# Kernel optimization log

Hardware: AMD Instinct MI355X
Metric: run time of the kernel (lower is better)

Reference implementation:

```python
import jax, jax.numpy as jnp
import numpy as np

B, C, H, W = 8, 512, 32, 32
N_HEADS = 4
D_K = C // N_HEADS  # 128


def setup_inputs() -> dict:
    key = jax.random.key(0)
    k1, k2, k3, k4, k5 = jax.random.split(key, 5)
    x = jax.random.normal(k1, (B, C, H, W), dtype=jnp.float32)
    # projection: Linear(in_ch, n_heads*d_k*3)
    Wp = jax.random.normal(k2, (C, N_HEADS * D_K * 3), dtype=jnp.float32) * (C ** -0.5)
    bp = jax.random.normal(k3, (N_HEADS * D_K * 3,), dtype=jnp.float32) * 0.01
    # output: Linear(n_heads*d_k, in_ch)
    Wo = jax.random.normal(k4, (N_HEADS * D_K, C), dtype=jnp.float32) * ((N_HEADS * D_K) ** -0.5)
    bo = jax.random.normal(k5, (C,), dtype=jnp.float32) * 0.01
    return {"x": x, "Wp": Wp, "bp": bp, "Wo": Wo, "bo": bo}


def reference(x, Wp, bp, Wo, bo):
    b, c, h, w = x.shape
    scale = D_K ** -0.5
    # [B, C, H, W] -> [B, N, C], N = H*W
    xs = x.reshape(b, c, h * w).transpose(0, 2, 1)
    qkv = (xs @ Wp + bp).reshape(b, h * w, N_HEADS, 3 * D_K)
    q, k, v = jnp.split(qkv, 3, axis=-1)  # each [B, N, H, D]
    attn = jnp.einsum('bihd,bjhd->bijh', q, k) * scale
    attn = jax.nn.softmax(attn, axis=2)  # softmax over j (keys)
    out = jnp.einsum('bijh,bjhd->bihd', attn, v)
    out = out.reshape(b, h * w, N_HEADS * D_K)
    out = out @ Wo + bo
    out = out + xs  # residual (note: GroupNorm is unused in the original forward)
    return out.transpose(0, 2, 1).reshape(b, c, h, w)
```

## Files before the change

### kernel.cpp

```cpp
#include <hip/hip_runtime.h>

#define NB 8
#define NC 512
#define NTOK 1024
#define NHEADS 4
#define DKH 128

typedef unsigned short u16;
typedef __attribute__((ext_vector_type(8))) short bf16x8;
typedef __attribute__((ext_vector_type(4))) float f32x4;

__device__ inline u16 f2b(float f) {
    union { float f; unsigned u; } v; v.f = f;
    unsigned r = v.u + 0x7fffu + ((v.u >> 16) & 1u);
    return (u16)(r >> 16);
}

__device__ __forceinline__ void gll16(const u16* g, u16* l) {
    __builtin_amdgcn_global_load_lds((const __attribute__((address_space(1))) unsigned*)g,
                                     (__attribute__((address_space(3))) unsigned*)l, 16, 0, 0);
}

__global__ __launch_bounds__(256) void prep(const float* __restrict__ x, const float* __restrict__ Wp,
                                            const float* __restrict__ Wo,
                                            u16* __restrict__ xsb, u16* __restrict__ WpT, u16* __restrict__ WoT)
{
    __shared__ float tile[32][33];
    const int z = blockIdx.z;
    const float* src; u16* dst; int R, Cc;
    if (z == 0)      { src = Wp; dst = WpT; R = 512; Cc = 1536; }
    else if (z == 1) { if (blockIdx.x >= 16) return; src = Wo; dst = WoT; R = 512; Cc = 512; }
    else             { if (blockIdx.x >= 32) return;
                       src = x + (long)(z-2)*NC*NTOK; dst = xsb + (long)(z-2)*NTOK*NC; R = NC; Cc = NTOK; }
    int c0 = blockIdx.x * 32, r0 = blockIdx.y * 32;
    int tx = threadIdx.x, ty = threadIdx.y;
    #pragma unroll
    for (int k = 0; k < 4; ++k)
        tile[ty + 8*k][tx] = src[(long)(r0 + ty + 8*k) * Cc + c0 + tx];
    __syncthreads();
    #pragma unroll
    for (int k = 0; k < 4; ++k)
        dst[(long)(c0 + ty + 8*k) * R + r0 + tx] = f2b(tile[tx][ty + 8*k]);
}

__global__ __launch_bounds__(256) void gemm_qkv(const u16* __restrict__ WpT, const u16* __restrict__ xsb,
                                                const float* __restrict__ bp,
                                                u16* __restrict__ qg, u16* __restrict__ kg, u16* __restrict__ vg)
{
    __shared__ union SmU {
        struct { u16 As[128][64]; u16 Bs[128][64]; } s;
        u16 Os[4][64][72];
    } sm;
    const int tid = threadIdx.x;
    const int m0 = blockIdx.x * 128;
    const int n0 = blockIdx.y * 128;
    const int w = tid >> 6, lane = tid & 63, quad = lane >> 4, lc = lane & 15;
    const int mo = (w & 1) * 64, no = (w >> 1) * 64;
    const int sw8 = (((lane & 7) ^ (lane >> 3)) << 3);
    const int xs = lc & 7;

    f32x4 acc[4][4] = {};

    for (int k0 = 0; k0 < NC; k0 += 64) {
        __syncthreads();
        #pragma unroll
        for (int p = 0; p < 4; ++p) {
            int row = w*32 + p*8 + (lane >> 3);
            gll16(&WpT[(long)(m0 + row) * NC + k0 + sw8], &sm.s.As[w*32 + p*8][0]);
            gll16(&xsb[(long)(n0 + row) * NC + k0 + sw8], &sm.s.Bs[w*32 + p*8][0]);
        }
        __syncthreads();
        #pragma unroll
        for (int ks = 0; ks < 2; ++ks) {
            bf16x8 af[4], bfr[4];
            #pragma unroll
            for (int t = 0; t < 4; ++t) {
                af[t]  = *(const bf16x8*)&sm.s.As[mo + t*16 + lc][((ks*4 + quad) ^ xs) << 3];
                bfr[t] = *(const bf16x8*)&sm.s.Bs[no + t*16 + lc][((ks*4 + quad) ^ xs) << 3];
            }
            #pragma unroll
            for (int mt = 0; mt < 4; ++mt)
                #pragma unroll
                for (int nt = 0; nt < 4; ++nt)
                    acc[mt][nt] = __builtin_amdgcn_mfma_f32_16x16x32_bf16(af[mt], bfr[nt], acc[mt][nt], 0, 0, 0);
        }
    }
    __syncthreads();

    const int bb = n0 >> 10;
    const int nblk = n0 & 1023;
    const int cqb = m0 + mo;
    const int h = cqb / 384;
    const int rem = cqb - h * 384;
    const int sel = rem >> 7;
    const int d_base = rem & 127;

    #pragma unroll
    for (int mt = 0; mt < 4; ++mt) {
        int cq0 = cqb + mt*16 + quad*4;
        float b0 = bp[cq0+0], b1 = bp[cq0+1], b2 = bp[cq0+2], b3 = bp[cq0+3];
        #pragma unroll
        for (int nt = 0; nt < 4; ++nt) {
            f32x4 a = acc[mt][nt];
            int nl = nt*16 + lc;
            int ml = mt*16 + quad*4;
            u16 e0 = f2b(a[0]+b0), e1 = f2b(a[1]+b1), e2 = f2b(a[2]+b2), e3 = f2b(a[3]+b3);
            if (sel == 2) {
                sm.Os[w][ml+0][nl] = e0; sm.Os[w][ml+1][nl] = e1;
                sm.Os[w][ml+2][nl] = e2; sm.Os[w][ml+3][nl] = e3;
            } else {
                sm.Os[w][nl][ml+0] = e0; sm.Os[w][nl][ml+1] = e1;
                sm.Os[w][nl][ml+2] = e2; sm.Os[w][nl][ml+3] = e3;
            }
        }
    }
    __builtin_amdgcn_sched_barrier(0);

    const long bhbase = (long)(bb * NHEADS + h);
    const int sw = sw8;
    if (sel == 2) {
        #pragma unroll
        for (int pass = 0; pass < 8; ++pass) {
            int ml  = pass*8 + (lane >> 3);
            int nl0 = (lane & 7) * 8;
            bf16x8 vv = *(const bf16x8*)&sm.Os[w][ml][nl0];
            *(bf16x8*)&vg[((bhbase*DKH + d_base + ml) << 10) + nblk + no + sw] = vv;
        }
    } else if (sel == 1) {
        #pragma unroll
        for (int pass = 0; pass < 8; ++pass) {
            int nl  = pass*8 + (lane >> 3);
            int ml0 = (lane & 7) * 8;
            bf16x8 vv = *(const bf16x8*)&sm.Os[w][nl][ml0];
            *(bf16x8*)&kg[((bhbase*NTOK + nblk + no + nl) << 7) + d_base + sw] = vv;
        }
    } else {
        #pragma unroll
        for (int pass = 0; pass < 8; ++pass) {
            int nl  = pass*8 + (lane >> 3);
            int ml0 = (lane & 7) * 8;
            bf16x8 vv = *(const bf16x8*)&sm.Os[w][nl][ml0];
            *(bf16x8*)&qg[((bhbase*NTOK + nblk + no + nl) << 7) + d_base + ml0] = vv;
        }
    }
}

__global__ __launch_bounds__(512) void attn(const u16* __restrict__ qg, const u16* __restrict__ kg,
                                            const u16* __restrict__ vtg, u16* __restrict__ ho)
{
    __shared__ u16 Ks[2][64*128];
    __shared__ u16 Vt[2][128*64];
    __shared__ u16 Ps[8][16][72];
    const int tid = threadIdx.x;
    const int w = tid >> 6, lane = tid & 63, quad = lane >> 4, lc = lane & 15;
    const int id = blockIdx.x;
    const int xcd = id & 7, rest = id >> 3, sub = rest & 3, bx = rest >> 2;
    const int pr = xcd + sub*8;
    const int b = pr >> 2, h = pr & 3;
    const int i0 = bx*128 + w*16;
    const long bh = (long)(b * NHEADS + h) << 17;
    const u16* qb = qg + bh;
    const u16* kb = kg + bh;
    const u16* vb = vtg + bh;
    const float SL2E = 0.08838834764831845f * 1.4426950408889634f;

    bf16x8 qf[4];
    #pragma unroll
    for (int ks = 0; ks < 4; ++ks)
        qf[ks] = *(const bf16x8*)&qb[(long)(i0 + lc) * DKH + ks*32 + quad*8];

    f32x4 o[8] = {};
    float lsum = 0.f;
    const int xs = lc & 7;

    #pragma unroll
    for (int p = 0; p < 2; ++p) {
        int ck = (w*2 + p)*64 + lane;
        gll16(&kb[(long)ck * 8], &Ks[0][(w*2 + p)*512]);
        gll16(&vb[(((long)(ck >> 3)) << 10) + (ck & 7)*8], &Vt[0][(w*2 + p)*512]);
    }

    for (int t = 0; t < 16; ++t) {
        __syncthreads();
        if (t < 15) {
            long jo = (long)(t+1) * 64;
            #pragma unroll
            for (int p = 0; p < 2; ++p) {
                int ck = (w*2 + p)*64 + lane;
                gll16(&kb[jo*128 + (long)ck*8], &Ks[(t+1)&1][(w*2 + p)*512]);
                gll16(&vb[(((long)(ck >> 3)) << 10) + jo + (ck & 7)*8], &Vt[(t+1)&1][(w*2 + p)*512]);
            }
        }
        const u16* K = Ks[t&1];
        const u16* V = Vt[t&1];

        f32x4 s[4] = {};
        #pragma unroll
        for (int ks = 0; ks < 4; ++ks)
            #pragma unroll
            for (int jt = 0; jt < 4; ++jt) {
                bf16x8 kf = *(const bf16x8*)&K[(jt*16 + lc)*128 + (((ks*4 + quad) ^ xs) << 3)];
                s[jt] = __builtin_amdgcn_mfma_f32_16x16x32_bf16(kf, qf[ks], s[jt], 0, 0, 0);
            }

        #pragma unroll
        for (int jt = 0; jt < 4; ++jt) {
            float p0 = __builtin_amdgcn_exp2f(s[jt][0] * SL2E);
            float p1 = __builtin_amdgcn_exp2f(s[jt][1] * SL2E);
            float p2 = __builtin_amdgcn_exp2f(s[jt][2] * SL2E);
            float p3 = __builtin_amdgcn_exp2f(s[jt][3] * SL2E);
            lsum += (p0 + p1) + (p2 + p3);
            ushort4 pk;
            pk.x = f2b(p0); pk.y = f2b(p1); pk.z = f2b(p2); pk.w = f2b(p3);
            *(ushort4*)&Ps[w][lc][jt*16 + quad*4] = pk;
        }
        __builtin_amdgcn_sched_barrier(0);

        #pragma unroll
        for (int ks2 = 0; ks2 < 2; ++ks2) {
            bf16x8 pf = *(const bf16x8*)&Ps[w][lc][ks2*32 + quad*8];
            #pragma unroll
            for (int dt = 0; dt < 8; ++dt) {
                bf16x8 vf = *(const bf16x8*)&V[(dt*16 + lc)*64 + (((ks2*4 + quad) ^ xs) << 3)];
                o[dt] = __builtin_amdgcn_mfma_f32_16x16x32_bf16(vf, pf, o[dt], 0, 0, 0);
            }
        }
    }

    lsum += __shfl_xor(lsum, 16);
    lsum += __shfl_xor(lsum, 32);
    float inv = 1.0f / lsum;

    #pragma unroll
    for (int dt = 0; dt < 8; ++dt) {
        ushort4 pk;
        pk.x = f2b(o[dt][0] * inv); pk.y = f2b(o[dt][1] * inv);
        pk.z = f2b(o[dt][2] * inv); pk.w = f2b(o[dt][3] * inv);
        *(ushort4*)&ho[(long)(b*NTOK + i0 + lc) * NC + h*DKH + dt*16 + quad*4] = pk;
    }
}

__global__ __launch_bounds__(256) void gemm_out(const u16* __restrict__ WoT, const u16* __restrict__ ho,
                                                const float* __restrict__ bo, const float* __restrict__ xin,
                                                float* __restrict__ dout)
{
    __shared__ struct { u16 As[128][64]; u16 Bs[64][64]; } sm;
    const int tid = threadIdx.x;
    const int m0 = blockIdx.x * 128;
    const int n0 = blockIdx.y * 64;
    const int w = tid >> 6, lane = tid & 63, quad = lane >> 4, lc = lane & 15;
    const int mo = (w & 1) * 64, no = (w >> 1) * 32;
    const int sw8 = (((lane & 7) ^ (lane >> 3)) << 3);
    const int xs = lc & 7;

    f32x4 acc[4][2] = {};

    for (int k0 = 0; k0 < NC; k0 += 64) {
        __syncthreads();
        #pragma unroll
        for (int p = 0; p < 4; ++p) {
            int row = w*32 + p*8 + (lane >> 3);
            gll16(&WoT[(long)(m0 + row) * NC + k0 + sw8], &sm.As[w*32 + p*8][0]);
        }
        #pragma unroll
        for (int p = 0; p < 2; ++p) {
            int row = w*16 + p*8 + (lane >> 3);
            gll16(&ho[(long)(n0 + row) * NC + k0 + sw8], &sm.Bs[w*16 + p*8][0]);
        }
        __syncthreads();
        #pragma unroll
        for (int ks = 0; ks < 2; ++ks) {
            bf16x8 af[4], bfr[2];
            #pragma unroll
            for (int t = 0; t < 4; ++t)
                af[t] = *(const bf16x8*)&sm.As[mo + t*16 + lc][((ks*4 + quad) ^ xs) << 3];
            #pragma unroll
            for (int t = 0; t < 2; ++t)
                bfr[t] = *(const bf16x8*)&sm.Bs[no + t*16 + lc][((ks*4 + quad) ^ xs) << 3];
            #pragma unroll
            for (int mt = 0; mt < 4; ++mt)
                #pragma unroll
                for (int nt = 0; nt < 2; ++nt)
                    acc[mt][nt] = __builtin_amdgcn_mfma_f32_16x16x32_bf16(af[mt], bfr[nt], acc[mt][nt], 0, 0, 0);
        }
    }

    const int bb = n0 >> 10;
    #pragma unroll
    for (int mt = 0; mt < 4; ++mt) {
        int cc0 = m0 + mo + mt*16 + quad*4;
        float b0 = bo[cc0+0], b1 = bo[cc0+1], b2 = bo[cc0+2], b3 = bo[cc0+3];
        #pragma unroll
        for (int nt = 0; nt < 2; ++nt) {
            int nl = (n0 + no + nt*16 + lc) & (NTOK - 1);
            f32x4 a = acc[mt][nt];
            long ix = ((long)(bb*NC + cc0) << 10) + nl;
            dout[ix]             = a[0] + b0 + xin[ix];
            dout[ix + (1 << 10)] = a[1] + b1 + xin[ix + (1 << 10)];
            dout[ix + (2 << 10)] = a[2] + b2 + xin[ix + (2 << 10)];
            dout[ix + (3 << 10)] = a[3] + b3 + xin[ix + (3 << 10)];
        }
    }
}

extern "C" void kernel_launch(void* const* d_in, const int* in_sizes, int n_in,
                              void* d_out, int out_size, void* d_ws, size_t ws_size,
                              hipStream_t stream)
{
    (void)in_sizes; (void)n_in; (void)out_size; (void)ws_size;
    const float* x  = (const float*)d_in[0];
    const float* Wp = (const float*)d_in[1];
    const float* bp = (const float*)d_in[2];
    const float* Wo = (const float*)d_in[3];
    const float* bo = (const float*)d_in[4];
    float* out = (float*)d_out;

    u16* ws  = (u16*)d_ws;
    u16* xsb = ws;
    u16* WpT = xsb + (long)NB * NTOK * NC;
    u16* WoT = WpT + 1536L * 512;
    u16* qg  = WoT + 512L * 512;
    u16* kg  = qg + (long)NB * NHEADS * NTOK * DKH;
    u16* vtg = kg + (long)NB * NHEADS * NTOK * DKH;
    u16* ho  = vtg + (long)NB * NHEADS * NTOK * DKH;

    prep<<<dim3(48, 16, 10), dim3(32, 8), 0, stream>>>(x, Wp, Wo, xsb, WpT, WoT);
    gemm_qkv<<<dim3(1536/128, (NB*NTOK)/128), 256, 0, stream>>>(WpT, xsb, bp, qg, kg, vtg);
    attn<<<dim3(256), 512, 0, stream>>>(qg, kg, vtg, ho);
    gemm_out<<<dim3(NC/128, (NB*NTOK)/64), 256, 0, stream>>>(WoT, ho, bo, x, out);
}
```

Baseline: 140.2 us.

## Process two query tiles per wave in attention to reuse K/V fragments

Attention blocks drop from 8 to 4 waves, and each wave now handles 32 query rows (two 16-row tiles). Each K and V fragment read from LDS feeds two MFMAs, which halves LDS traffic per unit of compute. The P buffer gets an XOR swizzle in place of padding, and s_setprio raises wave priority around the MFMA sections. In exchange it uses more registers per wave, leaves fewer waves per block to hide latency, and with the grid unchanged gives fewer total waves.

```diff
diff --git a/kernel.cpp b/kernel.cpp
--- a/kernel.cpp
+++ b/kernel.cpp
@@ -145,39 +145,42 @@
     }
 }
 
-__global__ __launch_bounds__(512) void attn(const u16* __restrict__ qg, const u16* __restrict__ kg,
-                                            const u16* __restrict__ vtg, u16* __restrict__ ho)
+__global__ __launch_bounds__(256, 2) void attn(const u16* __restrict__ qg, const u16* __restrict__ kg,
+                                               const u16* __restrict__ vtg, u16* __restrict__ ho)
 {
     __shared__ u16 Ks[2][64*128];
     __shared__ u16 Vt[2][128*64];
-    __shared__ u16 Ps[8][16][72];
+    __shared__ u16 Ps[4][32][64];
     const int tid = threadIdx.x;
     const int w = tid >> 6, lane = tid & 63, quad = lane >> 4, lc = lane & 15;
     const int id = blockIdx.x;
     const int xcd = id & 7, rest = id >> 3, sub = rest & 3, bx = rest >> 2;
     const int pr = xcd + sub*8;
     const int b = pr >> 2, h = pr & 3;
-    const int i0 = bx*128 + w*16;
+    const int i0 = bx*128 + w*32;
     const long bh = (long)(b * NHEADS + h) << 17;
     const u16* qb = qg + bh;
     const u16* kb = kg + bh;
     const u16* vb = vtg + bh;
     const float SL2E = 0.08838834764831845f * 1.4426950408889634f;
 
-    bf16x8 qf[4];
-    #pragma unroll
-    for (int ks = 0; ks < 4; ++ks)
-        qf[ks] = *(const bf16x8*)&qb[(long)(i0 + lc) * DKH + ks*32 + quad*8];
-
-    f32x4 o[8] = {};
-    float lsum = 0.f;
+    bf16x8 qf[2][4];
+    #pragma unroll
+    for (int it = 0; it < 2; ++it)
+        #pragma unroll
+        for (int ks = 0; ks < 4; ++ks)
+            qf[it][ks] = *(const bf16x8*)&qb[(long)(i0 + it*16 + lc) * DKH + ks*32 + quad*8];
+
+    f32x4 o[2][8] = {};
+    float lsum0 = 0.f, lsum1 = 0.f;
     const int xs = lc & 7;
-
-    #pragma unroll
-    for (int p = 0; p < 2; ++p) {
-        int ck = (w*2 + p)*64 + lane;
-        gll16(&kb[(long)ck * 8], &Ks[0][(w*2 + p)*512]);
-        gll16(&vb[(((long)(ck >> 3)) << 10) + (ck & 7)*8], &Vt[0][(w*2 + p)*512]);
+    const int psw = (lc & 7) << 3;
+
+    #pragma unroll
+    for (int p = 0; p < 4; ++p) {
+        int ck = (w*4 + p)*64 + lane;
+        gll16(&kb[(long)ck * 8], &Ks[0][(w*4 + p)*512]);
+        gll16(&vb[(((long)(ck >> 3)) << 10) + (ck & 7)*8], &Vt[0][(w*4 + p)*512]);
     }
 
     for (int t = 0; t < 16; ++t) {
@@ -185,58 +188,75 @@
         if (t < 15) {
             long jo = (long)(t+1) * 64;
             #pragma unroll
-            for (int p = 0; p < 2; ++p) {
-                int ck = (w*2 + p)*64 + lane;
-                gll16(&kb[jo*128 + (long)ck*8], &Ks[(t+1)&1][(w*2 + p)*512]);
-                gll16(&vb[(((long)(ck >> 3)) << 10) + jo + (ck & 7)*8], &Vt[(t+1)&1][(w*2 + p)*512]);
+            for (int p = 0; p < 4; ++p) {
+                int ck = (w*4 + p)*64 + lane;
+                gll16(&kb[jo*128 + (long)ck*8], &Ks[(t+1)&1][(w*4 + p)*512]);
+                gll16(&vb[(((long)(ck >> 3)) << 10) + jo + (ck & 7)*8], &Vt[(t+1)&1][(w*4 + p)*512]);
             }
         }
         const u16* K = Ks[t&1];
         const u16* V = Vt[t&1];
 
-        f32x4 s[4] = {};
+        f32x4 s[2][4] = {};
+        __builtin_amdgcn_s_setprio(1);
         #pragma unroll
         for (int ks = 0; ks < 4; ++ks)
             #pragma unroll
             for (int jt = 0; jt < 4; ++jt) {
                 bf16x8 kf = *(const bf16x8*)&K[(jt*16 + lc)*128 + (((ks*4 + quad) ^ xs) << 3)];
-                s[jt] = __builtin_amdgcn_mfma_f32_16x16x32_bf16(kf, qf[ks], s[jt], 0, 0, 0);
-            }
-
-        #pragma unroll
-        for (int jt = 0; jt < 4; ++jt) {
-            float p0 = __builtin_amdgcn_exp2f(s[jt][0] * SL2E);
-            float p1 = __builtin_amdgcn_exp2f(s[jt][1] * SL2E);
-            float p2 = __builtin_amdgcn_exp2f(s[jt][2] * SL2E);
-            float p3 = __builtin_amdgcn_exp2f(s[jt][3] * SL2E);
-            lsum += (p0 + p1) + (p2 + p3);
-            ushort4 pk;
-            pk.x = f2b(p0); pk.y = f2b(p1); pk.z = f2b(p2); pk.w = f2b(p3);
-            *(ushort4*)&Ps[w][lc][jt*16 + quad*4] = pk;
-        }
+                s[0][jt] = __builtin_amdgcn_mfma_f32_16x16x32_bf16(kf, qf[0][ks], s[0][jt], 0, 0, 0);
+                s[1][jt] = __builtin_amdgcn_mfma_f32_16x16x32_bf16(kf, qf[1][ks], s[1][jt], 0, 0, 0);
+            }
+        __builtin_amdgcn_s_setprio(0);
+
+        #pragma unroll
+        for (int it = 0; it < 2; ++it)
+            #pragma unroll
+            for (int jt = 0; jt < 4; ++jt) {
+                float p0 = __builtin_amdgcn_exp2f(s[it][jt][0] * SL2E);
+                float p1 = __builtin_amdgcn_exp2f(s[it][jt][1] * SL2E);
+                float p2 = __builtin_amdgcn_exp2f(s[it][jt][2] * SL2E);
+                float p3 = __builtin_amdgcn_exp2f(s[it][jt][3] * SL2E);
+                if (it == 0) lsum0 += (p0 + p1) + (p2 + p3);
+                else         lsum1 += (p0 + p1) + (p2 + p3);
+                ushort4 pk;
+                pk.x = f2b(p0); pk.y = f2b(p1); pk.z = f2b(p2); pk.w = f2b(p3);
+                *(ushort4*)&Ps[w][it*16 + lc][(jt*16 + quad*4) ^ psw] = pk;
+            }
         __builtin_amdgcn_sched_barrier(0);
 
+        __builtin_amdgcn_s_setprio(1);
         #pragma unroll
         for (int ks2 = 0; ks2 < 2; ++ks2) {
-            bf16x8 pf = *(const bf16x8*)&Ps[w][lc][ks2*32 + quad*8];
+            bf16x8 pf0 = *(const bf16x8*)&Ps[w][lc]     [(ks2*32 + quad*8) ^ psw];
+            bf16x8 pf1 = *(const bf16x8*)&Ps[w][16 + lc][(ks2*32 + quad*8) ^ psw];
             #pragma unroll
             for (int dt = 0; dt < 8; ++dt) {
                 bf16x8 vf = *(const bf16x8*)&V[(dt*16 + lc)*64 + (((ks2*4 + quad) ^ xs) << 3)];
-                o[dt] = __builtin_amdgcn_mfma_f32_16x16x32_bf16(vf, pf, o[dt], 0, 0, 0);
-            }
-        }
-    }
-
-    lsum += __shfl_xor(lsum, 16);
-    lsum += __shfl_xor(lsum, 32);
-    float inv = 1.0f / lsum;
+                o[0][dt] = __builtin_amdgcn_mfma_f32_16x16x32_bf16(vf, pf0, o[0][dt], 0, 0, 0);
+                o[1][dt] = __builtin_amdgcn_mfma_f32_16x16x32_bf16(vf, pf1, o[1][dt], 0, 0, 0);
+            }
+        }
+        __builtin_amdgcn_s_setprio(0);
+    }
+
+    lsum0 += __shfl_xor(lsum0, 16);
+    lsum0 += __shfl_xor(lsum0, 32);
+    lsum1 += __shfl_xor(lsum1, 16);
+    lsum1 += __shfl_xor(lsum1, 32);
+    float inv0 = 1.0f / lsum0;
+    float inv1 = 1.0f / lsum1;
 
     #pragma unroll
     for (int dt = 0; dt < 8; ++dt) {
         ushort4 pk;
-        pk.x = f2b(o[dt][0] * inv); pk.y = f2b(o[dt][1] * inv);
-        pk.z = f2b(o[dt][2] * inv); pk.w = f2b(o[dt][3] * inv);
+        pk.x = f2b(o[0][dt][0] * inv0); pk.y = f2b(o[0][dt][1] * inv0);
+        pk.z = f2b(o[0][dt][2] * inv0); pk.w = f2b(o[0][dt][3] * inv0);
         *(ushort4*)&ho[(long)(b*NTOK + i0 + lc) * NC + h*DKH + dt*16 + quad*4] = pk;
+        ushort4 pk1;
+        pk1.x = f2b(o[1][dt][0] * inv1); pk1.y = f2b(o[1][dt][1] * inv1);
+        pk1.z = f2b(o[1][dt][2] * inv1); pk1.w = f2b(o[1][dt][3] * inv1);
+        *(ushort4*)&ho[(long)(b*NTOK + i0 + 16 + lc) * NC + h*DKH + dt*16 + quad*4] = pk1;
     }
 }
 
@@ -326,6 +346,6 @@
 
     prep<<<dim3(48, 16, 10), dim3(32, 8), 0, stream>>>(x, Wp, Wo, xsb, WpT, WoT);
     gemm_qkv<<<dim3(1536/128, (NB*NTOK)/128), 256, 0, stream>>>(WpT, xsb, bp, qg, kg, vtg);
-    attn<<<dim3(256), 512, 0, stream>>>(qg, kg, vtg, ho);
+    attn<<<dim3(256), 256, 0, stream>>>(qg, kg, vtg, ho);
     gemm_out<<<dim3(NC/128, (NB*NTOK)/64), 256, 0, stream>>>(WoT, ho, bo, x, out);
 }
```

Result: slower. 145.4 us (+3.7%).

## Enlarge QKV GEMM tiles to 256x256 with double-buffered LDS and XCD remap

Applied to the files above, without the earlier changes.

The QKV projection GEMM moves from 128x128 tiles with 256 threads to 256x256 tiles with 512 threads, so each wave computes 128x64 outputs. Global-to-LDS loads are now double-buffered, with vmcnt waits and raw barriers so the next K slice loads while the current one is multiplied, and MFMA sections raise wave priority. Block IDs are remapped across XCDs, and the epilogue writes Q, K and V in two 64-row halves. The goal is more operand reuse and hidden load latency. The cost is that only 192 blocks remain for the whole GPU, and 128KB of LDS limits each CU to one block.

```diff
diff --git a/kernel.cpp b/kernel.cpp
--- a/kernel.cpp
+++ b/kernel.cpp
@@ -43,105 +43,131 @@
         dst[(long)(c0 + ty + 8*k) * R + r0 + tx] = f2b(tile[tx][ty + 8*k]);
 }
 
-__global__ __launch_bounds__(256) void gemm_qkv(const u16* __restrict__ WpT, const u16* __restrict__ xsb,
-                                                const float* __restrict__ bp,
-                                                u16* __restrict__ qg, u16* __restrict__ kg, u16* __restrict__ vg)
+__global__ __launch_bounds__(512, 2) void gemm_qkv(const u16* __restrict__ WpT, const u16* __restrict__ xsb,
+                                                   const float* __restrict__ bp,
+                                                   u16* __restrict__ qg, u16* __restrict__ kg, u16* __restrict__ vg)
 {
     __shared__ union SmU {
-        struct { u16 As[128][64]; u16 Bs[128][64]; } s;
-        u16 Os[4][64][72];
+        struct { u16 As[2][256][64]; u16 Bs[2][256][64]; } s;
+        u16 Os[8][64][72];
     } sm;
     const int tid = threadIdx.x;
-    const int m0 = blockIdx.x * 128;
-    const int n0 = blockIdx.y * 128;
+    const int raw = blockIdx.x;
+    const int L = (raw & 7) * 24 + (raw >> 3);
+    const int mb = L % 6, nb = L / 6;
+    const int m0 = mb * 256;
+    const int n0 = nb * 256;
     const int w = tid >> 6, lane = tid & 63, quad = lane >> 4, lc = lane & 15;
-    const int mo = (w & 1) * 64, no = (w >> 1) * 64;
+    const int mo = (w & 1) * 128, no = (w >> 1) * 64;
     const int sw8 = (((lane & 7) ^ (lane >> 3)) << 3);
-    const int xs = lc & 7;
-
-    f32x4 acc[4][4] = {};
-
-    for (int k0 = 0; k0 < NC; k0 += 64) {
-        __syncthreads();
-        #pragma unroll
-        for (int p = 0; p < 4; ++p) {
-            int row = w*32 + p*8 + (lane >> 3);
-            gll16(&WpT[(long)(m0 + row) * NC + k0 + sw8], &sm.s.As[w*32 + p*8][0]);
-            gll16(&xsb[(long)(n0 + row) * NC + k0 + sw8], &sm.s.Bs[w*32 + p*8][0]);
-        }
-        __syncthreads();
+    const int xs = lc & 15 & 7;
+    const int srow = (lane >> 3);
+
+    f32x4 acc[8][4] = {};
+
+    #pragma unroll
+    for (int p = 0; p < 4; ++p) {
+        int row = w*32 + p*8 + srow;
+        gll16(&WpT[(long)(m0 + row) * NC + 0 + sw8], &sm.s.As[0][w*32 + p*8][0]);
+        gll16(&xsb[(long)(n0 + row) * NC + 0 + sw8], &sm.s.Bs[0][w*32 + p*8][0]);
+    }
+
+    for (int t = 0; t < 8; ++t) {
+        if (t < 7) {
+            const long kk = (long)(t + 1) * 64;
+            const int nbuf = (t + 1) & 1;
+            #pragma unroll
+            for (int p = 0; p < 4; ++p) {
+                int row = w*32 + p*8 + srow;
+                gll16(&WpT[(long)(m0 + row) * NC + kk + sw8], &sm.s.As[nbuf][w*32 + p*8][0]);
+                gll16(&xsb[(long)(n0 + row) * NC + kk + sw8], &sm.s.Bs[nbuf][w*32 + p*8][0]);
+            }
+            asm volatile("s_waitcnt vmcnt(8)" ::: "memory");
+        } else {
+            asm volatile("s_waitcnt vmcnt(0)" ::: "memory");
+        }
+        __builtin_amdgcn_s_barrier();
+        __builtin_amdgcn_sched_barrier(0);
+
+        const int cb = t & 1;
         #pragma unroll
         for (int ks = 0; ks < 2; ++ks) {
-            bf16x8 af[4], bfr[4];
-            #pragma unroll
-            for (int t = 0; t < 4; ++t) {
-                af[t]  = *(const bf16x8*)&sm.s.As[mo + t*16 + lc][((ks*4 + quad) ^ xs) << 3];
-                bfr[t] = *(const bf16x8*)&sm.s.Bs[no + t*16 + lc][((ks*4 + quad) ^ xs) << 3];
-            }
-            #pragma unroll
-            for (int mt = 0; mt < 4; ++mt)
+            bf16x8 af[8], bfr[4];
+            #pragma unroll
+            for (int mt = 0; mt < 8; ++mt)
+                af[mt] = *(const bf16x8*)&sm.s.As[cb][mo + mt*16 + lc][((ks*4 + quad) ^ xs) << 3];
+            #pragma unroll
+            for (int nt = 0; nt < 4; ++nt)
+                bfr[nt] = *(const bf16x8*)&sm.s.Bs[cb][no + nt*16 + lc][((ks*4 + quad) ^ xs) << 3];
+            __builtin_amdgcn_s_setprio(1);
+            #pragma unroll
+            for (int mt = 0; mt < 8; ++mt)
                 #pragma unroll
                 for (int nt = 0; nt < 4; ++nt)
                     acc[mt][nt] = __builtin_amdgcn_mfma_f32_16x16x32_bf16(af[mt], bfr[nt], acc[mt][nt], 0, 0, 0);
-        }
-    }
-    __syncthreads();
+            __builtin_amdgcn_s_setprio(0);
+        }
+        __builtin_amdgcn_s_barrier();
+    }
 
     const int bb = n0 >> 10;
     const int nblk = n0 & 1023;
-    const int cqb = m0 + mo;
-    const int h = cqb / 384;
-    const int rem = cqb - h * 384;
-    const int sel = rem >> 7;
-    const int d_base = rem & 127;
-
-    #pragma unroll
-    for (int mt = 0; mt < 4; ++mt) {
-        int cq0 = cqb + mt*16 + quad*4;
-        float b0 = bp[cq0+0], b1 = bp[cq0+1], b2 = bp[cq0+2], b3 = bp[cq0+3];
-        #pragma unroll
-        for (int nt = 0; nt < 4; ++nt) {
-            f32x4 a = acc[mt][nt];
-            int nl = nt*16 + lc;
-            int ml = mt*16 + quad*4;
-            u16 e0 = f2b(a[0]+b0), e1 = f2b(a[1]+b1), e2 = f2b(a[2]+b2), e3 = f2b(a[3]+b3);
-            if (sel == 2) {
-                sm.Os[w][ml+0][nl] = e0; sm.Os[w][ml+1][nl] = e1;
-                sm.Os[w][ml+2][nl] = e2; sm.Os[w][ml+3][nl] = e3;
-            } else {
-                sm.Os[w][nl][ml+0] = e0; sm.Os[w][nl][ml+1] = e1;
-                sm.Os[w][nl][ml+2] = e2; sm.Os[w][nl][ml+3] = e3;
-            }
-        }
-    }
-    __builtin_amdgcn_sched_barrier(0);
-
+    const int pb = (m0 + mo) >> 7;
+    const int h = pb / 3;
+    const int sel = pb % 3;
     const long bhbase = (long)(bb * NHEADS + h);
-    const int sw = sw8;
-    if (sel == 2) {
-        #pragma unroll
-        for (int pass = 0; pass < 8; ++pass) {
-            int ml  = pass*8 + (lane >> 3);
-            int nl0 = (lane & 7) * 8;
-            bf16x8 vv = *(const bf16x8*)&sm.Os[w][ml][nl0];
-            *(bf16x8*)&vg[((bhbase*DKH + d_base + ml) << 10) + nblk + no + sw] = vv;
-        }
-    } else if (sel == 1) {
-        #pragma unroll
-        for (int pass = 0; pass < 8; ++pass) {
-            int nl  = pass*8 + (lane >> 3);
-            int ml0 = (lane & 7) * 8;
-            bf16x8 vv = *(const bf16x8*)&sm.Os[w][nl][ml0];
-            *(bf16x8*)&kg[((bhbase*NTOK + nblk + no + nl) << 7) + d_base + sw] = vv;
-        }
-    } else {
-        #pragma unroll
-        for (int pass = 0; pass < 8; ++pass) {
-            int nl  = pass*8 + (lane >> 3);
-            int ml0 = (lane & 7) * 8;
-            bf16x8 vv = *(const bf16x8*)&sm.Os[w][nl][ml0];
-            *(bf16x8*)&qg[((bhbase*NTOK + nblk + no + nl) << 7) + d_base + ml0] = vv;
-        }
+
+    #pragma unroll
+    for (int mh = 0; mh < 2; ++mh) {
+        const int d0 = mh * 64;
+        #pragma unroll
+        for (int mt4 = 0; mt4 < 4; ++mt4) {
+            int mt = mh*4 + mt4;
+            int cq0 = m0 + mo + mt*16 + quad*4;
+            float b0 = bp[cq0+0], b1 = bp[cq0+1], b2 = bp[cq0+2], b3 = bp[cq0+3];
+            #pragma unroll
+            for (int nt = 0; nt < 4; ++nt) {
+                f32x4 a = acc[mt][nt];
+                int nl = nt*16 + lc;
+                int ml = mt4*16 + quad*4;
+                u16 e0 = f2b(a[0]+b0), e1 = f2b(a[1]+b1), e2 = f2b(a[2]+b2), e3 = f2b(a[3]+b3);
+                if (sel == 2) {
+                    sm.Os[w][ml+0][nl] = e0; sm.Os[w][ml+1][nl] = e1;
+                    sm.Os[w][ml+2][nl] = e2; sm.Os[w][ml+3][nl] = e3;
+                } else {
+                    sm.Os[w][nl][ml+0] = e0; sm.Os[w][nl][ml+1] = e1;
+                    sm.Os[w][nl][ml+2] = e2; sm.Os[w][nl][ml+3] = e3;
+                }
+            }
+        }
+        __builtin_amdgcn_sched_barrier(0);
+
+        if (sel == 2) {
+            #pragma unroll
+            for (int pass = 0; pass < 8; ++pass) {
+                int ml  = pass*8 + srow;
+                int nl0 = (lane & 7) * 8;
+                bf16x8 vv = *(const bf16x8*)&sm.Os[w][ml][nl0];
+                *(bf16x8*)&vg[((bhbase*DKH + d0 + ml) << 10) + nblk + no + sw8] = vv;
+            }
+        } else if (sel == 1) {
+            #pragma unroll
+            for (int pass = 0; pass < 8; ++pass) {
+                int nl  = pass*8 + srow;
+                int ml0 = (lane & 7) * 8;
+                bf16x8 vv = *(const bf16x8*)&sm.Os[w][nl][ml0];
+                *(bf16x8*)&kg[((bhbase*NTOK + nblk + no + nl) << 7) + d0 + sw8] = vv;
+            }
+        } else {
+            #pragma unroll
+            for (int pass = 0; pass < 8; ++pass) {
+                int nl  = pass*8 + srow;
+                int ml0 = (lane & 7) * 8;
+                bf16x8 vv = *(const bf16x8*)&sm.Os[w][nl][ml0];
+                *(bf16x8*)&qg[((bhbase*NTOK + nblk + no + nl) << 7) + d0 + ml0] = vv;
+            }
+        }
+        __builtin_amdgcn_sched_barrier(0);
     }
 }
 
@@ -325,7 +351,7 @@
     u16* ho  = vtg + (long)NB * NHEADS * NTOK * DKH;
 
     prep<<<dim3(48, 16, 10), dim3(32, 8), 0, stream>>>(x, Wp, Wo, xsb, WpT, WoT);
-    gemm_qkv<<<dim3(1536/128, (NB*NTOK)/128), 256, 0, stream>>>(WpT, xsb, bp, qg, kg, vtg);
+    gemm_qkv<<<dim3(192), 512, 0, stream>>>(WpT, xsb, bp, qg, kg, vtg);
     attn<<<dim3(256), 512, 0, stream>>>(qg, kg, vtg, ho);
     gemm_out<<<dim3(NC/128, (NB*NTOK)/64), 256, 0, stream>>>(WoT, ho, bo, x, out);
 }
```

Measured after the change: 141.5 us. Within noise of the previous version (+1.0%).
